# Kernel tuning notes

Measured on AMD Instinct MI355X. Metric: run time of the kernel, lower is better.

Reference implementation:

```python
import jax, jax.numpy as jnp
import numpy as np

B = 262144
G = 3           # n_goods
HDIM = 256
IN = G * 2 + 1  # 7


def setup_inputs() -> dict:
    key = jax.random.key(0)
    ks = jax.random.split(key, 10)
    inp = {
        "log_p": jax.random.normal(ks[0], (B, G), jnp.float32),
        "log_y": jax.random.normal(ks[1], (B, 1), jnp.float32),
        "log_xb_prev": jax.random.normal(ks[2], (B, G), jnp.float32),
        "log_q_prev": jax.random.normal(ks[3], (B, G), jnp.float32),
        # Linear weights stored torch-style: (out, in)
        "W1": jax.random.normal(ks[4], (HDIM, IN), jnp.float32) * np.sqrt(2.0 / IN),
        "b1": jnp.zeros((HDIM,), jnp.float32),
        "W2": jax.random.normal(ks[5], (HDIM, HDIM), jnp.float32) * np.sqrt(2.0 / HDIM),
        "b2": jnp.zeros((HDIM,), jnp.float32),
        "W3": jax.random.normal(ks[6], (HDIM // 2, HDIM), jnp.float32) * np.sqrt(2.0 / HDIM),
        "b3": jnp.zeros((HDIM // 2,), jnp.float32),
        "W4": jax.random.uniform(ks[7], (G, HDIM // 2), jnp.float32,
                                  minval=-0.1 * np.sqrt(6.0 / (G + HDIM // 2)),
                                  maxval=0.1 * np.sqrt(6.0 / (G + HDIM // 2))),
        "b4": jnp.zeros((G,), jnp.float32),
        "log_beta": jnp.float32(1.5),
        "log_delta": jnp.float32(np.log(0.7 / 0.3)),
    }
    return inp


def reference(log_p, log_y, log_xb_prev, log_q_prev,
              W1, b1, W2, b2, W3, b3, W4, b4, log_beta, log_delta):
    beta = jnp.clip(jnp.exp(log_beta), 0.5, 20.0)
    delta = jax.nn.sigmoid(log_delta)
    xb = delta * log_xb_prev + (1.0 - delta) * log_q_prev      # (B, G)
    x = jnp.concatenate([log_p, log_y, xb], axis=1)            # (B, 2G+1)
    h = jax.nn.silu(x @ W1.T + b1)                             # (B, 256)
    h = jax.nn.silu(h @ W2.T + b2)                             # (B, 256)
    h = jax.nn.silu(h @ W3.T + b3)                             # (B, 128)
    logits = (h @ W4.T + b4) * beta                            # (B, G)
    return jax.nn.softmax(logits, axis=1)
```

## Files before the change

### kernel.cpp

```cpp
#include <hip/hip_runtime.h>
#include <hip/hip_bf16.h>

#define B_TOTAL 262144
#define G 3
#define HD 256
#define HD2 128
#define ROWS 64
#define LDH 264

typedef short short8 __attribute__((ext_vector_type(8)));
typedef float floatx4 __attribute__((ext_vector_type(4)));

__device__ __forceinline__ unsigned short f2bf(float f) {
    unsigned u = __builtin_bit_cast(unsigned, f);
    u += 0x7FFFu + ((u >> 16) & 1u);
    return (unsigned short)(u >> 16);
}

__device__ __forceinline__ unsigned pack_bf16x2(float a, float b) {
#if __has_builtin(__builtin_amdgcn_cvt_pk_bf16_f32)
    auto r = __builtin_amdgcn_cvt_pk_bf16_f32(a, b);
    unsigned u;
    __builtin_memcpy(&u, &r, 4);
    return u;
#else
    return (unsigned)f2bf(a) | ((unsigned)f2bf(b) << 16);
#endif
}

__device__ __forceinline__ float fast_rcp(float x) {
#if __has_builtin(__builtin_amdgcn_rcpf)
    return __builtin_amdgcn_rcpf(x);
#else
    return 1.0f / x;
#endif
}
__device__ __forceinline__ float silu_f(float x) {
    return x * fast_rcp(1.0f + __expf(-x));
}

__global__ void convert_w_kernel(const float* __restrict__ W1, const float* __restrict__ W2,
                                 const float* __restrict__ W3, const float* __restrict__ W4,
                                 unsigned short* __restrict__ w1bf, unsigned short* __restrict__ w2bf,
                                 unsigned short* __restrict__ w3bf, unsigned short* __restrict__ w4bf) {
    int i = blockIdx.x * 256 + threadIdx.x;
    if (i < HD * HD)  w2bf[i] = f2bf(W2[i]);
    if (i < HD2 * HD) w3bf[i] = f2bf(W3[i]);
    if (i < HD * 32) { int r = i >> 5, k = i & 31; w1bf[i] = (k < 7) ? f2bf(W1[r * 7 + k]) : (unsigned short)0; }
    if (i < 16 * HD2) { int r = i >> 7, k = i & 127; w4bf[i] = (r < G) ? f2bf(W4[r * HD2 + k]) : (unsigned short)0; }
}

__global__ __launch_bounds__(256, 3) void mlp_kernel(
    const float* __restrict__ log_p, const float* __restrict__ log_y,
    const float* __restrict__ log_xb, const float* __restrict__ log_q,
    const float* __restrict__ b1, const float* __restrict__ b2,
    const float* __restrict__ b3, const float* __restrict__ b4,
    const float* __restrict__ p_log_beta, const float* __restrict__ p_log_delta,
    const unsigned short* __restrict__ w1bf, const unsigned short* __restrict__ w2bf,
    const unsigned short* __restrict__ w3bf, const unsigned short* __restrict__ w4bf,
    float* __restrict__ out)
{
    __shared__ __align__(16) unsigned short hA[ROWS][LDH];
    __shared__ __align__(16) unsigned short x_bf[ROWS][32];
    __shared__ __align__(16) float bias1_s[HD];
    __shared__ __align__(16) float bias2_s[HD];
    __shared__ __align__(16) float bias3_s[HD2];

    const int tid  = threadIdx.x;
    const int lane = tid & 63;
    const int wv   = tid >> 6;
    const int quad = lane >> 4;
    const int l15  = lane & 15;
    const int row0 = blockIdx.x * ROWS;

    const float beta  = fminf(fmaxf(__expf(p_log_beta[0]), 0.5f), 20.0f);
    const float delta = fast_rcp(1.0f + __expf(-p_log_delta[0]));

    bias1_s[tid] = b1[tid];
    bias2_s[tid] = b2[tid];
    if (tid < HD2) bias3_s[tid] = b3[tid];
    if (tid < ROWS) {
        const int r = row0 + tid;
        const float p0 = log_p[r * 3 + 0], p1 = log_p[r * 3 + 1], p2 = log_p[r * 3 + 2];
        const float y  = log_y[r];
        const float xb0 = delta * log_xb[r * 3 + 0] + (1.0f - delta) * log_q[r * 3 + 0];
        const float xb1 = delta * log_xb[r * 3 + 1] + (1.0f - delta) * log_q[r * 3 + 1];
        const float xb2 = delta * log_xb[r * 3 + 2] + (1.0f - delta) * log_q[r * 3 + 2];
        uint4 u0;
        u0.x = pack_bf16x2(p0, p1);
        u0.y = pack_bf16x2(p2, y);
        u0.z = pack_bf16x2(xb0, xb1);
        u0.w = pack_bf16x2(xb2, 0.0f);
        const uint4 uz = {0u, 0u, 0u, 0u};
        *(uint4*)&x_bf[tid][0]  = u0;
        *(uint4*)&x_bf[tid][8]  = uz;
        *(uint4*)&x_bf[tid][16] = uz;
        *(uint4*)&x_bf[tid][24] = uz;
    }
    __syncthreads();

    #define EPILOGUE(ACC, M, N0)                                                   \
        {                                                                          \
            const float v0 = silu_f((ACC)[0]);                                     \
            const float v1 = silu_f((ACC)[1]);                                     \
            const float v2 = silu_f((ACC)[2]);                                     \
            const float v3 = silu_f((ACC)[3]);                                     \
            uint2 u; u.x = pack_bf16x2(v0, v1); u.y = pack_bf16x2(v2, v3);         \
            *(uint2*)&hA[(M)][(N0)] = u;                                           \
        }

    {
        const int nbase = wv * 64;
        short8 aw[4], bx[4];
        #pragma unroll
        for (int nt = 0; nt < 4; ++nt)
            aw[nt] = *(const short8*)(w1bf + (nbase + nt * 16 + l15) * 32 + quad * 8);
        #pragma unroll
        for (int mt = 0; mt < 4; ++mt)
            bx[mt] = *(const short8*)&x_bf[mt * 16 + l15][quad * 8];
        #pragma unroll
        for (int nt = 0; nt < 4; ++nt) {
            const float4 bv = *(const float4*)&bias1_s[nbase + nt * 16 + quad * 4];
            #pragma unroll
            for (int mt = 0; mt < 4; ++mt) {
                floatx4 acc = (floatx4){bv.x, bv.y, bv.z, bv.w};
                acc = __builtin_amdgcn_mfma_f32_16x16x32_bf16(aw[nt], bx[mt], acc, 0, 0, 0);
                EPILOGUE(acc, mt * 16 + l15, nbase + nt * 16 + quad * 4);
            }
        }
    }
    __syncthreads();

    {
        const int nbase = wv * 64;
        floatx4 acc[4][4];
        #pragma unroll
        for (int nt = 0; nt < 4; ++nt) {
            const float4 bv = *(const float4*)&bias2_s[nbase + nt * 16 + quad * 4];
            #pragma unroll
            for (int mt = 0; mt < 4; ++mt)
                acc[mt][nt] = (floatx4){bv.x, bv.y, bv.z, bv.w};
        }
        short8 aw[2][4], bh[2][4];
        #pragma unroll
        for (int nt = 0; nt < 4; ++nt)
            aw[0][nt] = *(const short8*)(w2bf + (nbase + nt * 16 + l15) * HD + quad * 8);
        #pragma unroll
        for (int mt = 0; mt < 4; ++mt)
            bh[0][mt] = *(const short8*)&hA[mt * 16 + l15][quad * 8];
        #pragma unroll
        for (int ks = 0; ks < 8; ++ks) {
            const int cur = ks & 1, nxt = cur ^ 1;
            if (ks < 7) {
                const int kb = (ks + 1) * 32 + quad * 8;
                #pragma unroll
                for (int nt = 0; nt < 4; ++nt)
                    aw[nxt][nt] = *(const short8*)(w2bf + (nbase + nt * 16 + l15) * HD + kb);
                #pragma unroll
                for (int mt = 0; mt < 4; ++mt)
                    bh[nxt][mt] = *(const short8*)&hA[mt * 16 + l15][kb];
            }
            #pragma unroll
            for (int mt = 0; mt < 4; ++mt)
                #pragma unroll
                for (int nt = 0; nt < 4; ++nt)
                    acc[mt][nt] = __builtin_amdgcn_mfma_f32_16x16x32_bf16(aw[cur][nt], bh[cur][mt], acc[mt][nt], 0, 0, 0);
        }
        __syncthreads();
        #pragma unroll
        for (int mt = 0; mt < 4; ++mt) {
            #pragma unroll
            for (int nt = 0; nt < 4; ++nt)
                EPILOGUE(acc[mt][nt], mt * 16 + l15, nbase + nt * 16 + quad * 4);
        }
    }
    __syncthreads();

    {
        const int nbase = wv * 32;
        floatx4 acc[4][2];
        #pragma unroll
        for (int nt = 0; nt < 2; ++nt) {
            const float4 bv = *(const float4*)&bias3_s[nbase + nt * 16 + quad * 4];
            #pragma unroll
            for (int mt = 0; mt < 4; ++mt)
                acc[mt][nt] = (floatx4){bv.x, bv.y, bv.z, bv.w};
        }
        short8 aw[2][2], bh[2][4];
        #pragma unroll
        for (int nt = 0; nt < 2; ++nt)
            aw[0][nt] = *(const short8*)(w3bf + (nbase + nt * 16 + l15) * HD + quad * 8);
        #pragma unroll
        for (int mt = 0; mt < 4; ++mt)
            bh[0][mt] = *(const short8*)&hA[mt * 16 + l15][quad * 8];
        #pragma unroll
        for (int ks = 0; ks < 8; ++ks) {
            const int cur = ks & 1, nxt = cur ^ 1;
            if (ks < 7) {
                const int kb = (ks + 1) * 32 + quad * 8;
                #pragma unroll
                for (int nt = 0; nt < 2; ++nt)
                    aw[nxt][nt] = *(const short8*)(w3bf + (nbase + nt * 16 + l15) * HD + kb);
                #pragma unroll
                for (int mt = 0; mt < 4; ++mt)
                    bh[nxt][mt] = *(const short8*)&hA[mt * 16 + l15][kb];
            }
            #pragma unroll
            for (int mt = 0; mt < 4; ++mt)
                #pragma unroll
                for (int nt = 0; nt < 2; ++nt)
                    acc[mt][nt] = __builtin_amdgcn_mfma_f32_16x16x32_bf16(aw[cur][nt], bh[cur][mt], acc[mt][nt], 0, 0, 0);
        }
        __syncthreads();
        #pragma unroll
        for (int mt = 0; mt < 4; ++mt) {
            #pragma unroll
            for (int nt = 0; nt < 2; ++nt)
                EPILOGUE(acc[mt][nt], mt * 16 + l15, nbase + nt * 16 + quad * 4);
        }
    }
    __syncthreads();

    {
        floatx4 acc;
        #pragma unroll
        for (int i = 0; i < 4; ++i) {
            const int rrow = quad * 4 + i;
            acc[i] = (rrow < G) ? b4[rrow] : 0.0f;
        }
        #pragma unroll
        for (int ks = 0; ks < 4; ++ks) {
            const int kb = ks * 32 + quad * 8;
            const short8 aw = *(const short8*)(w4bf + l15 * HD2 + kb);
            const short8 bh = *(const short8*)&hA[wv * 16 + l15][kb];
            acc = __builtin_amdgcn_mfma_f32_16x16x32_bf16(aw, bh, acc, 0, 0, 0);
        }
        if (lane < 16) {
            const float l0 = acc[0] * beta;
            const float l1 = acc[1] * beta;
            const float l2 = acc[2] * beta;
            const float m  = fmaxf(l0, fmaxf(l1, l2));
            const float e0 = __expf(l0 - m), e1 = __expf(l1 - m), e2 = __expf(l2 - m);
            const float inv = fast_rcp(e0 + e1 + e2);
            const int r = row0 + wv * 16 + l15;
            out[r * 3 + 0] = e0 * inv;
            out[r * 3 + 1] = e1 * inv;
            out[r * 3 + 2] = e2 * inv;
        }
    }
    #undef EPILOGUE
}

extern "C" void kernel_launch(void* const* d_in, const int* in_sizes, int n_in,
                              void* d_out, int out_size, void* d_ws, size_t ws_size,
                              hipStream_t stream) {
    (void)in_sizes; (void)n_in; (void)out_size; (void)ws_size;
    const float* log_p  = (const float*)d_in[0];
    const float* log_y  = (const float*)d_in[1];
    const float* log_xb = (const float*)d_in[2];
    const float* log_q  = (const float*)d_in[3];
    const float* W1 = (const float*)d_in[4];
    const float* b1 = (const float*)d_in[5];
    const float* W2 = (const float*)d_in[6];
    const float* b2 = (const float*)d_in[7];
    const float* W3 = (const float*)d_in[8];
    const float* b3 = (const float*)d_in[9];
    const float* W4 = (const float*)d_in[10];
    const float* b4 = (const float*)d_in[11];
    const float* lb = (const float*)d_in[12];
    const float* ld = (const float*)d_in[13];

    unsigned short* w2bf = (unsigned short*)d_ws;
    unsigned short* w3bf = w2bf + HD * HD;
    unsigned short* w1bf = w3bf + HD2 * HD;
    unsigned short* w4bf = w1bf + HD * 32;

    convert_w_kernel<<<256, 256, 0, stream>>>(W1, W2, W3, W4, w1bf, w2bf, w3bf, w4bf);
    mlp_kernel<<<B_TOTAL / ROWS, 256, 0, stream>>>(
        log_p, log_y, log_xb, log_q, b1, b2, b3, b4, lb, ld,
        w1bf, w2bf, w3bf, w4bf, (float*)d_out);
}
```

Measured before the change: 192.6 us.

## Give each wave its own row slab in layer 3 and drop barriers

Layer 3 is re-partitioned so each wave computes all 128 outputs for its own 16 rows, instead of 32 outputs for all 64 rows. Each wave then reads and overwrites only its own rows of the shared activation buffer, so the barriers before the layer-3 epilogue and before layer 4 are removed. The trade-off is that every wave now fetches the whole W3 weight tile from global/L2 (four times the per-wave weight loads) while issuing fewer shared-memory activation reads. Launch bounds also rise from 3 to 4 blocks per CU, which constrains register allocation to allow higher occupancy.

```diff
diff --git a/kernel.cpp b/kernel.cpp
--- a/kernel.cpp
+++ b/kernel.cpp
@@ -50,7 +50,7 @@
     if (i < 16 * HD2) { int r = i >> 7, k = i & 127; w4bf[i] = (r < G) ? f2bf(W4[r * HD2 + k]) : (unsigned short)0; }
 }
 
-__global__ __launch_bounds__(256, 3) void mlp_kernel(
+__global__ __launch_bounds__(256, 4) void mlp_kernel(
     const float* __restrict__ log_p, const float* __restrict__ log_y,
     const float* __restrict__ log_xb, const float* __restrict__ log_q,
     const float* __restrict__ b1, const float* __restrict__ b2,
@@ -177,49 +177,35 @@
     __syncthreads();
 
     {
-        const int nbase = wv * 32;
-        floatx4 acc[4][2];
-        #pragma unroll
-        for (int nt = 0; nt < 2; ++nt) {
-            const float4 bv = *(const float4*)&bias3_s[nbase + nt * 16 + quad * 4];
-            #pragma unroll
-            for (int mt = 0; mt < 4; ++mt)
-                acc[mt][nt] = (floatx4){bv.x, bv.y, bv.z, bv.w};
-        }
-        short8 aw[2][2], bh[2][4];
-        #pragma unroll
-        for (int nt = 0; nt < 2; ++nt)
-            aw[0][nt] = *(const short8*)(w3bf + (nbase + nt * 16 + l15) * HD + quad * 8);
-        #pragma unroll
-        for (int mt = 0; mt < 4; ++mt)
-            bh[0][mt] = *(const short8*)&hA[mt * 16 + l15][quad * 8];
+        floatx4 acc[8];
+        #pragma unroll
+        for (int nt = 0; nt < 8; ++nt) {
+            const float4 bv = *(const float4*)&bias3_s[nt * 16 + quad * 4];
+            acc[nt] = (floatx4){bv.x, bv.y, bv.z, bv.w};
+        }
+        short8 aw[2][8], bh[2];
+        #pragma unroll
+        for (int nt = 0; nt < 8; ++nt)
+            aw[0][nt] = *(const short8*)(w3bf + (nt * 16 + l15) * HD + quad * 8);
+        bh[0] = *(const short8*)&hA[wv * 16 + l15][quad * 8];
         #pragma unroll
         for (int ks = 0; ks < 8; ++ks) {
             const int cur = ks & 1, nxt = cur ^ 1;
             if (ks < 7) {
                 const int kb = (ks + 1) * 32 + quad * 8;
                 #pragma unroll
-                for (int nt = 0; nt < 2; ++nt)
-                    aw[nxt][nt] = *(const short8*)(w3bf + (nbase + nt * 16 + l15) * HD + kb);
-                #pragma unroll
-                for (int mt = 0; mt < 4; ++mt)
-                    bh[nxt][mt] = *(const short8*)&hA[mt * 16 + l15][kb];
+                for (int nt = 0; nt < 8; ++nt)
+                    aw[nxt][nt] = *(const short8*)(w3bf + (nt * 16 + l15) * HD + kb);
+                bh[nxt] = *(const short8*)&hA[wv * 16 + l15][kb];
             }
             #pragma unroll
-            for (int mt = 0; mt < 4; ++mt)
-                #pragma unroll
-                for (int nt = 0; nt < 2; ++nt)
-                    acc[mt][nt] = __builtin_amdgcn_mfma_f32_16x16x32_bf16(aw[cur][nt], bh[cur][mt], acc[mt][nt], 0, 0, 0);
-        }
-        __syncthreads();
-        #pragma unroll
-        for (int mt = 0; mt < 4; ++mt) {
-            #pragma unroll
-            for (int nt = 0; nt < 2; ++nt)
-                EPILOGUE(acc[mt][nt], mt * 16 + l15, nbase + nt * 16 + quad * 4);
-        }
-    }
-    __syncthreads();
+            for (int nt = 0; nt < 8; ++nt)
+                acc[nt] = __builtin_amdgcn_mfma_f32_16x16x32_bf16(aw[cur][nt], bh[cur], acc[nt], 0, 0, 0);
+        }
+        #pragma unroll
+        for (int nt = 0; nt < 8; ++nt)
+            EPILOGUE(acc[nt], wv * 16 + l15, nt * 16 + quad * 4);
+    }
 
     {
         floatx4 acc;
@@ -231,9 +217,9 @@
         #pragma unroll
         for (int ks = 0; ks < 4; ++ks) {
             const int kb = ks * 32 + quad * 8;
-            const short8 aw = *(const short8*)(w4bf + l15 * HD2 + kb);
-            const short8 bh = *(const short8*)&hA[wv * 16 + l15][kb];
-            acc = __builtin_amdgcn_mfma_f32_16x16x32_bf16(aw, bh, acc, 0, 0, 0);
+            const short8 aw4 = *(const short8*)(w4bf + l15 * HD2 + kb);
+            const short8 bh4 = *(const short8*)&hA[wv * 16 + l15][kb];
+            acc = __builtin_amdgcn_mfma_f32_16x16x32_bf16(aw4, bh4, acc, 0, 0, 0);
         }
         if (lane < 16) {
             const float l0 = acc[0] * beta;
```

After: 271.2 us. 40.8% more time.
